# Kernel tuning notes

Measured on AMD Instinct MI355X. Metric: run time of the kernel, lower is better.

The kernel has to match this reference:

```python
import jax, jax.numpy as jnp
import numpy as np

DIM = 1024
N_HEADS = 16
HEAD_DIM = DIM // N_HEADS
SCALE = HEAD_DIM ** -0.5


def setup_inputs() -> dict:
    key = jax.random.key(0)
    kx, kq, kk, kv = jax.random.split(key, 4)
    x = jax.random.normal(kx, (2, 2048, DIM), dtype=jnp.float32)
    bv_q = jax.random.normal(kq, (N_HEADS, HEAD_DIM), dtype=jnp.float32) * 0.02
    bv_k = jax.random.normal(kk, (N_HEADS, HEAD_DIM), dtype=jnp.float32) * 0.02
    bv_v = jax.random.normal(kv, (N_HEADS, HEAD_DIM), dtype=jnp.float32) * 0.02
    return {"x": x, "bv_q": bv_q, "bv_k": bv_k, "bv_v": bv_v}


def reference(x, bv_q, bv_k, bv_v):
    B, T, D = x.shape
    H, HD = N_HEADS, HEAD_DIM
    x_h = x.reshape(B, T, H, HD)
    # sign-gated Q/K/V (sign of binding vectors; elementwise +/-1 gating)
    Q = x_h * jnp.sign(bv_q)  # [B,T,H,HD]
    K = x_h * jnp.sign(bv_k)
    V = x_h * jnp.sign(bv_v)
    # causal scores, sigmoid gating (no softmax)
    scores = jnp.einsum('bqhd,bkhd->bhqk', Q, K) * SCALE  # [B,H,T,T]
    causal = jnp.tril(jnp.ones((T, T), dtype=bool))
    attn = jnp.where(causal, jax.nn.sigmoid(scores * 4.0), 0.0)
    out = jnp.einsum('bhqk,bkhd->bqhd', attn, V)  # [B,T,H,HD]
    return out.reshape(B, T, D)
```

## Files before the change

kernel.cpp:

```cpp
#include <hip/hip_runtime.h>
#include <hip/hip_bf16.h>
#include <stdint.h>

#define DIM 1024
#define T_LEN 2048
#define NB 2
#define NH 16
#define HD 64
#define NQT 32

typedef float f32x4 __attribute__((ext_vector_type(4)));
typedef float f32x16 __attribute__((ext_vector_type(16)));
typedef __bf16 bf16x8 __attribute__((ext_vector_type(8)));
typedef __bf16 bf16x2 __attribute__((ext_vector_type(2)));
typedef unsigned int u32;
typedef unsigned int u32x4 __attribute__((ext_vector_type(4)));

__device__ __forceinline__ float sgnf(float v) {
    return (v > 0.f) ? 1.f : ((v < 0.f) ? -1.f : 0.f);
}

__device__ __forceinline__ float sigmoid_half(float v) {
    return __builtin_amdgcn_rcpf(1.f + __builtin_amdgcn_exp2f(-0.72134752f * v));
}

__device__ __forceinline__ u32 pack2(float p0, float p1) {
    bf16x2 t = {(__bf16)p0, (__bf16)p1};
    return __builtin_bit_cast(u32, t);
}

__device__ __forceinline__ void gload16(const __bf16* g, __bf16* l) {
    __builtin_amdgcn_global_load_lds(
        (__attribute__((address_space(1))) void*)g,
        (__attribute__((address_space(3))) void*)l,
        16, 0, 0);
}

__global__ __launch_bounds__(256) void prep_kernel(
    const float* __restrict__ x, __bf16* __restrict__ xb, __bf16* __restrict__ xt)
{
    __shared__ __align__(16) __bf16 tile[64][72];

    const int bid = blockIdx.x;
    const int h = bid & 15, tmp = bid >> 4, tt = tmp & 31, b = tmp >> 5;
    const int tid = threadIdx.x;
    const int r = tid >> 2, c0 = (tid & 3) * 16;

    const size_t rowbase = ((size_t)(b * T_LEN + tt * 64 + r)) * DIM + h * HD + c0;
    const float* xp = x + rowbase;

    __bf16 v[16];
    #pragma unroll
    for (int i = 0; i < 16; i += 4) {
        f32x4 f = *(const f32x4*)(xp + i);
        #pragma unroll
        for (int j = 0; j < 4; ++j) v[i + j] = (__bf16)f[j];
    }
    bf16x8 s0, s1;
    #pragma unroll
    for (int j = 0; j < 8; ++j) { s0[j] = v[j]; s1[j] = v[8 + j]; }
    *(bf16x8*)(xb + rowbase)     = s0;
    *(bf16x8*)(xb + rowbase + 8) = s1;
    *(bf16x8*)&tile[r][c0]     = s0;
    *(bf16x8*)&tile[r][c0 + 8] = s1;

    __syncthreads();

    const int d = tid >> 2, t0c = (tid & 3) * 16;
    __bf16 ov[16];
    #pragma unroll
    for (int i = 0; i < 16; ++i) ov[i] = tile[t0c + i][d];
    bf16x8 o0, o1;
    #pragma unroll
    for (int j = 0; j < 8; ++j) { o0[j] = ov[j]; o1[j] = ov[8 + j]; }
    const size_t obase = ((size_t)((b * NH + h) * HD + d)) * T_LEN + tt * 64 + t0c;
    *(bf16x8*)(xt + obase)     = o0;
    *(bf16x8*)(xt + obase + 8) = o1;
}

__global__ __launch_bounds__(256, 4) void mba_main(
    const __bf16* __restrict__ xb, const __bf16* __restrict__ xt,
    const float* __restrict__ bvq, const float* __restrict__ bvk,
    const float* __restrict__ bvv, float* __restrict__ out)
{
    __shared__ __align__(16) __bf16 Kb[3][64][64];
    __shared__ __align__(16) __bf16 Vb[2][64][64];

    const int bid = blockIdx.x;
    const int u = bid >> 5;
    const int jj = u >> 3, aa = u & 7;
    const int qt = 8 * jj + ((jj & 1) ? (7 - aa) : aa);
    const int bh = bid & 31;
    const int b = bh >> 4, h = bh & 15;
    const int q0 = qt * 64;

    const int tid = threadIdx.x;
    const int w = tid >> 6, l = tid & 63;
    const int c = l & 31, hi = l >> 5;
    const int qh = w & 1, sh = w >> 1;

    const size_t xb_bh = (size_t)b * T_LEN * DIM + h * HD;
    const size_t xt_bh = (size_t)((b * NH + h) * HD) * T_LEN;

    const int rr = l >> 3;
    const int sw = ((l & 7) ^ rr) << 3;

    auto STAGE_K = [&](int buf, int kvt) {
        const int kv0s = kvt * 64;
        #pragma unroll
        for (int pt = 0; pt < 2; ++pt) {
            const int r0 = w * 8 + pt * 32;
            gload16(xb + xb_bh + (size_t)(kv0s + r0 + rr) * DIM + sw, &Kb[buf][r0][0]);
        }
    };
    auto STAGE_V = [&](int buf, int kvt) {
        const int kv0s = kvt * 64;
        #pragma unroll
        for (int pt = 0; pt < 2; ++pt) {
            const int r0 = w * 8 + pt * 32;
            gload16(xt + xt_bh + (size_t)(r0 + rr) * T_LEN + kv0s + sw, &Vb[buf][r0][0]);
        }
    };

    STAGE_K(0, 0);
    STAGE_V(0, 0);
    if (qt >= 1) STAGE_K(1, 1);

    bf16x8 qa[4];
    {
        const float* bq = bvq + h * HD;
        const float* bk = bvk + h * HD;
        const int qrow = q0 + qh * 32 + c;
        #pragma unroll
        for (int m = 0; m < 4; ++m) {
            const int d0 = m * 16 + hi * 8;
            bf16x8 va = *(const bf16x8*)(xb + xb_bh + (size_t)qrow * DIM + d0);
            #pragma unroll
            for (int j = 0; j < 8; ++j) {
                float f = sgnf(bq[d0 + j]) * sgnf(bk[d0 + j]);
                qa[m][j] = (__bf16)((float)va[j] * f);
            }
        }
    }
    float sv[2];
    #pragma unroll
    for (int nd = 0; nd < 2; ++nd) sv[nd] = sgnf(bvv[h * HD + nd * 32 + c]);

    f32x16 o[2];
    #pragma unroll
    for (int nd = 0; nd < 2; ++nd)
        #pragma unroll
        for (int i = 0; i < 16; ++i) o[nd][i] = 0.f;

    int cur = 0;
    const int krow = sh * 32 + c;
    const int swz = (c & 7) << 4;

    for (int t = 0; t <= qt; ++t) {
        const bool last = (t == qt);
        if (last) { asm volatile("s_waitcnt vmcnt(0)" ::: "memory"); }
        else      { asm volatile("s_waitcnt vmcnt(2)" ::: "memory"); }
        __builtin_amdgcn_sched_barrier(0);
        __builtin_amdgcn_s_barrier();
        __builtin_amdgcn_sched_barrier(0);

        if (t + 1 <= qt) STAGE_V((t + 1) & 1, t + 1);
        __builtin_amdgcn_sched_barrier(0);
        if (t + 2 <= qt) {
            int stg = cur + 2; if (stg >= 3) stg -= 3;
            STAGE_K(stg, t + 2);
        }
        __builtin_amdgcn_sched_barrier(0);

        f32x16 ss;
        #pragma unroll
        for (int i = 0; i < 16; ++i) ss[i] = 0.f;
        #pragma unroll
        for (int m = 0; m < 4; ++m) {
            bf16x8 kf = *(const bf16x8*)((const char*)&Kb[cur][krow][0]
                          + ((m * 32 + hi * 16) ^ swz));
            ss = __builtin_amdgcn_mfma_f32_32x32x16_bf16(kf, qa[m], ss, 0, 0, 0);
        }

        u32 W[8];
        #pragma unroll
        for (int i = 0; i < 8; ++i) {
            const int r0 = 2 * i;
            const int sl = (r0 & 3) + 8 * (r0 >> 2) + 4 * hi;
            float p0 = sigmoid_half(ss[r0]);
            float p1 = sigmoid_half(ss[r0 + 1]);
            if (last) {
                const int sg = sh * 32 + sl;
                const int qg = qh * 32 + c;
                if (sg > qg)     p0 = 0.f;
                if (sg + 1 > qg) p1 = 0.f;
            }
            W[i] = pack2(p0, p1);
        }

        asm volatile("v_permlane32_swap_b32 %0, %1" : "+v"(W[0]), "+v"(W[2]));
        asm volatile("v_permlane32_swap_b32 %0, %1" : "+v"(W[1]), "+v"(W[3]));
        asm volatile("v_permlane32_swap_b32 %0, %1" : "+v"(W[4]), "+v"(W[6]));
        asm volatile("v_permlane32_swap_b32 %0, %1" : "+v"(W[5]), "+v"(W[7]));
        bf16x8 pa[2];
        pa[0] = __builtin_bit_cast(bf16x8, (u32x4){W[0], W[1], W[2], W[3]});
        pa[1] = __builtin_bit_cast(bf16x8, (u32x4){W[4], W[5], W[6], W[7]});

        #pragma unroll
        for (int m = 0; m < 2; ++m) {
            #pragma unroll
            for (int nd = 0; nd < 2; ++nd) {
                bf16x8 vf = *(const bf16x8*)((const char*)&Vb[t & 1][nd * 32 + c][0]
                              + ((sh * 64 + m * 32 + hi * 16) ^ swz));
                o[nd] = __builtin_amdgcn_mfma_f32_32x32x16_bf16(pa[m], vf, o[nd], 0, 0, 0);
            }
        }
        cur = (cur == 2) ? 0 : cur + 1;
    }

    __syncthreads();
    float (*osc)[64] = (float(*)[64]) & Kb[0][0][0];

    if (sh == 1) {
        #pragma unroll
        for (int r = 0; r < 16; ++r) {
            const int qloc = (r & 3) + 8 * (r >> 2) + 4 * hi;
            #pragma unroll
            for (int nd = 0; nd < 2; ++nd)
                osc[qh * 32 + qloc][nd * 32 + c] = o[nd][r];
        }
    }
    __syncthreads();
    if (sh == 0) {
        #pragma unroll
        for (int r = 0; r < 16; ++r) {
            const int qloc = (r & 3) + 8 * (r >> 2) + 4 * hi;
            const size_t row = (size_t)(b * T_LEN + q0 + qh * 32 + qloc) * DIM + h * HD;
            #pragma unroll
            for (int nd = 0; nd < 2; ++nd) {
                float val = (o[nd][r] + osc[qh * 32 + qloc][nd * 32 + c]) * sv[nd];
                out[row + nd * 32 + c] = val;
            }
        }
    }
}

__global__ __launch_bounds__(256) void mba_fallback(
    const float* __restrict__ x,
    const float* __restrict__ bvq,
    const float* __restrict__ bvk,
    const float* __restrict__ bvv,
    float* __restrict__ out)
{
    __shared__ __align__(16) __bf16 Kb[64][72];
    __shared__ __align__(16) __bf16 Vt[HD][72];
    __shared__ __align__(16) __bf16 Pb[4][16][72];

    const int bid = blockIdx.x;
    const int qt  = (NQT - 1) - (bid & (NQT - 1));
    const int bh  = bid >> 5;
    const int b   = bh >> 4;
    const int h   = bh & 15;

    const int tid = threadIdx.x;
    const int w   = tid >> 6;
    const int l   = tid & 63;
    const int lq  = l & 15;
    const int lh  = l >> 4;

    const int  q0    = qt * 64;
    const long xbase = ((long)b * T_LEN) * DIM + h * HD;

    bf16x8 qa[2];
    {
        const int   qrow = q0 + w * 16 + lq;
        const float* qp  = x + xbase + (long)qrow * DIM + lh * 8;
        const float* gp  = bvq + h * HD + lh * 8;
        #pragma unroll
        for (int ks = 0; ks < 2; ++ks)
            #pragma unroll
            for (int j = 0; j < 8; ++j)
                qa[ks][j] = (__bf16)(qp[ks * 32 + j] * sgnf(gp[ks * 32 + j]));
    }

    f32x4 o[4];
    #pragma unroll
    for (int n = 0; n < 4; ++n) o[n] = (f32x4){0.f, 0.f, 0.f, 0.f};

    const int r_st = tid >> 2;
    const int c0   = (tid & 3) * 16;
    const float* gk = bvk + h * HD + c0;
    const float* gv = bvv + h * HD + c0;

    for (int kvt = 0; kvt <= qt; ++kvt) {
        const int kv0 = kvt * 64;
        __syncthreads();
        {
            const float* kp = x + xbase + (long)(kv0 + r_st) * DIM + c0;
            __bf16 kb[16];
            #pragma unroll
            for (int i = 0; i < 16; ++i) kb[i] = (__bf16)(kp[i] * sgnf(gk[i]));
            *(bf16x8*)&Kb[r_st][c0]     = *(bf16x8*)&kb[0];
            *(bf16x8*)&Kb[r_st][c0 + 8] = *(bf16x8*)&kb[8];
            #pragma unroll
            for (int i = 0; i < 16; ++i)
                Vt[c0 + i][r_st] = (__bf16)(kp[i] * sgnf(gv[i]));
        }
        __syncthreads();

        f32x4 s[4];
        #pragma unroll
        for (int n = 0; n < 4; ++n) s[n] = (f32x4){0.f, 0.f, 0.f, 0.f};
        #pragma unroll
        for (int ks = 0; ks < 2; ++ks)
            #pragma unroll
            for (int n = 0; n < 4; ++n) {
                bf16x8 kf = *(const bf16x8*)&Kb[n * 16 + lq][ks * 32 + lh * 8];
                s[n] = __builtin_amdgcn_mfma_f32_16x16x32_bf16(qa[ks], kf, s[n], 0, 0, 0);
            }

        const bool diag = (kvt == qt);
        #pragma unroll
        for (int n = 0; n < 4; ++n)
            #pragma unroll
            for (int j = 0; j < 4; ++j) {
                float p = sigmoid_half(s[n][j]);
                if (diag && (n * 16 + lq) > (w * 16 + lh * 4 + j)) p = 0.f;
                Pb[w][lh * 4 + j][n * 16 + lq] = (__bf16)p;
            }

        #pragma unroll
        for (int ks = 0; ks < 2; ++ks) {
            bf16x8 pf = *(const bf16x8*)&Pb[w][lq][ks * 32 + lh * 8];
            #pragma unroll
            for (int n = 0; n < 4; ++n) {
                bf16x8 vf = *(const bf16x8*)&Vt[n * 16 + lq][ks * 32 + lh * 8];
                o[n] = __builtin_amdgcn_mfma_f32_16x16x32_bf16(pf, vf, o[n], 0, 0, 0);
            }
        }
    }

    float* op = out + ((long)b * T_LEN + q0 + w * 16) * DIM + h * HD;
    #pragma unroll
    for (int n = 0; n < 4; ++n)
        #pragma unroll
        for (int j = 0; j < 4; ++j)
            op[(long)(lh * 4 + j) * DIM + n * 16 + lq] = o[n][j];
}

extern "C" void kernel_launch(void* const* d_in, const int* in_sizes, int n_in,
                              void* d_out, int out_size, void* d_ws, size_t ws_size,
                              hipStream_t stream) {
    (void)in_sizes; (void)n_in; (void)out_size;
    const float* x   = (const float*)d_in[0];
    const float* bvq = (const float*)d_in[1];
    const float* bvk = (const float*)d_in[2];
    const float* bvv = (const float*)d_in[3];
    float* out = (float*)d_out;

    const size_t XB_BYTES = (size_t)NB * T_LEN * DIM * sizeof(__bf16);
    const size_t XT_BYTES = XB_BYTES;

    if (ws_size < XB_BYTES + XT_BYTES) {
        mba_fallback<<<NB * NH * NQT, 256, 0, stream>>>(x, bvq, bvk, bvv, out);
        return;
    }

    __bf16* xb = (__bf16*)d_ws;
    __bf16* xt = xb + (size_t)NB * T_LEN * DIM;

    prep_kernel<<<NB * NQT * NH, 256, 0, stream>>>(x, xb, xt);
    mba_main<<<NB * NH * NQT, 256, 0, stream>>>(xb, xt, bvq, bvk, bvv, out);
}
```

Baseline: 47.43 us.

## Split causal KV range into 4-tile chunks with atomic output accumulation

Each block now handles at most four KV tiles of one query tile rather than the whole causal prefix, so block work is balanced and 144 chunks per (b,h) are launched. Partial results are merged with float atomic adds into an output zeroed by a memset. The V sign gating moves into the prep kernel's transposed copy, and the in-block LDS reduction between the two key halves is dropped in favour of atomics. This trades the long-tail imbalance of the diagonal schedule for extra atomic traffic, a memset, and repeated Q loads per chunk.

```diff
diff --git a/kernel.cpp b/kernel.cpp
--- a/kernel.cpp
+++ b/kernel.cpp
@@ -8,6 +8,7 @@
 #define NH 16
 #define HD 64
 #define NQT 32
+#define NCHUNK 144
 
 typedef float f32x4 __attribute__((ext_vector_type(4)));
 typedef float f32x16 __attribute__((ext_vector_type(16)));
@@ -37,7 +38,8 @@
 }
 
 __global__ __launch_bounds__(256) void prep_kernel(
-    const float* __restrict__ x, __bf16* __restrict__ xb, __bf16* __restrict__ xt)
+    const float* __restrict__ x, const float* __restrict__ bvv,
+    __bf16* __restrict__ xb, __bf16* __restrict__ xt)
 {
     __shared__ __align__(16) __bf16 tile[64][72];
 
@@ -67,9 +69,10 @@
     __syncthreads();
 
     const int d = tid >> 2, t0c = (tid & 3) * 16;
+    const float g = sgnf(bvv[h * HD + d]);
     __bf16 ov[16];
     #pragma unroll
-    for (int i = 0; i < 16; ++i) ov[i] = tile[t0c + i][d];
+    for (int i = 0; i < 16; ++i) ov[i] = (__bf16)((float)tile[t0c + i][d] * g);
     bf16x8 o0, o1;
     #pragma unroll
     for (int j = 0; j < 8; ++j) { o0[j] = ov[j]; o1[j] = ov[8 + j]; }
@@ -81,15 +84,18 @@
 __global__ __launch_bounds__(256, 4) void mba_main(
     const __bf16* __restrict__ xb, const __bf16* __restrict__ xt,
     const float* __restrict__ bvq, const float* __restrict__ bvk,
-    const float* __restrict__ bvv, float* __restrict__ out)
+    float* __restrict__ out)
 {
     __shared__ __align__(16) __bf16 Kb[3][64][64];
     __shared__ __align__(16) __bf16 Vb[2][64][64];
 
     const int bid = blockIdx.x;
-    const int u = bid >> 5;
-    const int jj = u >> 3, aa = u & 7;
-    const int qt = 8 * jj + ((jj & 1) ? (7 - aa) : aa);
+    int rem = bid >> 5;
+    int qt = 31;
+    while (rem >= ((qt + 4) >> 2)) { rem -= (qt + 4) >> 2; --qt; }
+    const int c4 = rem * 4;
+    const int CL = min(4, qt + 1 - c4);
+
     const int bh = bid & 31;
     const int b = bh >> 4, h = bh & 15;
     const int q0 = qt * 64;
@@ -122,9 +128,9 @@
         }
     };
 
-    STAGE_K(0, 0);
-    STAGE_V(0, 0);
-    if (qt >= 1) STAGE_K(1, 1);
+    STAGE_K(0, c4);
+    STAGE_V(0, c4);
+    if (CL >= 2) STAGE_K(1, c4 + 1);
 
     bf16x8 qa[4];
     {
@@ -142,9 +148,6 @@
             }
         }
     }
-    float sv[2];
-    #pragma unroll
-    for (int nd = 0; nd < 2; ++nd) sv[nd] = sgnf(bvv[h * HD + nd * 32 + c]);
 
     f32x16 o[2];
     #pragma unroll
@@ -156,19 +159,21 @@
     const int krow = sh * 32 + c;
     const int swz = (c & 7) << 4;
 
-    for (int t = 0; t <= qt; ++t) {
-        const bool last = (t == qt);
-        if (last) { asm volatile("s_waitcnt vmcnt(0)" ::: "memory"); }
-        else      { asm volatile("s_waitcnt vmcnt(2)" ::: "memory"); }
+    for (int lt = 0; lt < CL; ++lt) {
+        const int gt = c4 + lt;
+        const bool last_local = (lt == CL - 1);
+        const bool diag = (gt == qt);
+        if (last_local) { asm volatile("s_waitcnt vmcnt(0)" ::: "memory"); }
+        else            { asm volatile("s_waitcnt vmcnt(2)" ::: "memory"); }
         __builtin_amdgcn_sched_barrier(0);
         __builtin_amdgcn_s_barrier();
         __builtin_amdgcn_sched_barrier(0);
 
-        if (t + 1 <= qt) STAGE_V((t + 1) & 1, t + 1);
+        if (lt + 1 < CL) STAGE_V((lt + 1) & 1, gt + 1);
         __builtin_amdgcn_sched_barrier(0);
-        if (t + 2 <= qt) {
+        if (lt + 2 < CL) {
             int stg = cur + 2; if (stg >= 3) stg -= 3;
-            STAGE_K(stg, t + 2);
+            STAGE_K(stg, gt + 2);
         }
         __builtin_amdgcn_sched_barrier(0);
 
@@ -189,7 +194,7 @@
             const int sl = (r0 & 3) + 8 * (r0 >> 2) + 4 * hi;
             float p0 = sigmoid_half(ss[r0]);
             float p1 = sigmoid_half(ss[r0 + 1]);
-            if (last) {
+            if (diag) {
                 const int sg = sh * 32 + sl;
                 const int qg = qh * 32 + c;
                 if (sg > qg)     p0 = 0.f;
@@ -210,7 +215,7 @@
         for (int m = 0; m < 2; ++m) {
             #pragma unroll
             for (int nd = 0; nd < 2; ++nd) {
-                bf16x8 vf = *(const bf16x8*)((const char*)&Vb[t & 1][nd * 32 + c][0]
+                bf16x8 vf = *(const bf16x8*)((const char*)&Vb[lt & 1][nd * 32 + c][0]
                               + ((sh * 64 + m * 32 + hi * 16) ^ swz));
                 o[nd] = __builtin_amdgcn_mfma_f32_32x32x16_bf16(pa[m], vf, o[nd], 0, 0, 0);
             }
@@ -218,30 +223,12 @@
         cur = (cur == 2) ? 0 : cur + 1;
     }
 
-    __syncthreads();
-    float (*osc)[64] = (float(*)[64]) & Kb[0][0][0];
-
-    if (sh == 1) {
-        #pragma unroll
-        for (int r = 0; r < 16; ++r) {
-            const int qloc = (r & 3) + 8 * (r >> 2) + 4 * hi;
-            #pragma unroll
-            for (int nd = 0; nd < 2; ++nd)
-                osc[qh * 32 + qloc][nd * 32 + c] = o[nd][r];
-        }
-    }
-    __syncthreads();
-    if (sh == 0) {
-        #pragma unroll
-        for (int r = 0; r < 16; ++r) {
-            const int qloc = (r & 3) + 8 * (r >> 2) + 4 * hi;
-            const size_t row = (size_t)(b * T_LEN + q0 + qh * 32 + qloc) * DIM + h * HD;
-            #pragma unroll
-            for (int nd = 0; nd < 2; ++nd) {
-                float val = (o[nd][r] + osc[qh * 32 + qloc][nd * 32 + c]) * sv[nd];
-                out[row + nd * 32 + c] = val;
-            }
-        }
+    #pragma unroll
+    for (int r = 0; r < 16; ++r) {
+        const int qloc = (r & 3) + 8 * (r >> 2) + 4 * hi;
+        float* op = out + (size_t)(b * T_LEN + q0 + qh * 32 + qloc) * DIM + h * HD + c;
+        unsafeAtomicAdd(op,      o[0][r]);
+        unsafeAtomicAdd(op + 32, o[1][r]);
     }
 }
 
@@ -351,7 +338,7 @@
 extern "C" void kernel_launch(void* const* d_in, const int* in_sizes, int n_in,
                               void* d_out, int out_size, void* d_ws, size_t ws_size,
                               hipStream_t stream) {
-    (void)in_sizes; (void)n_in; (void)out_size;
+    (void)in_sizes; (void)n_in;
     const float* x   = (const float*)d_in[0];
     const float* bvq = (const float*)d_in[1];
     const float* bvk = (const float*)d_in[2];
@@ -369,6 +356,7 @@
     __bf16* xb = (__bf16*)d_ws;
     __bf16* xt = xb + (size_t)NB * T_LEN * DIM;
 
-    prep_kernel<<<NB * NQT * NH, 256, 0, stream>>>(x, xb, xt);
-    mba_main<<<NB * NH * NQT, 256, 0, stream>>>(xb, xt, bvq, bvk, bvv, out);
-}
+    hipMemsetAsync(d_out, 0, (size_t)out_size * sizeof(float), stream);
+    prep_kernel<<<NB * NQT * NH, 256, 0, stream>>>(x, bvv, xb, xt);
+    mba_main<<<NCHUNK * 32, 256, 0, stream>>>(xb, xt, bvq, bvk, out);
+}
```

New measurement: 141.8 us. 2.99x slower.

## Pair complementary causal query tiles per block to share K/V staging

Applied to the files above, without the earlier changes.

Each block now processes two query tiles (qt and 31-qt) for the same batch-head, so every block does equal causal work and shares each staged K/V tile between both tiles' MFMAs. The grid is halved to 512 blocks and launch bounds relaxed to 2 waves per SIMD to make room for doubled accumulator registers. The V sign gating is folded into the prep transpose, which removes the per-output multiply. This trades occupancy and parallelism for load balance and halved K/V traffic.

```diff
diff --git a/kernel.cpp b/kernel.cpp
--- a/kernel.cpp
+++ b/kernel.cpp
@@ -37,7 +37,8 @@
 }
 
 __global__ __launch_bounds__(256) void prep_kernel(
-    const float* __restrict__ x, __bf16* __restrict__ xb, __bf16* __restrict__ xt)
+    const float* __restrict__ x, const float* __restrict__ bvv,
+    __bf16* __restrict__ xb, __bf16* __restrict__ xt)
 {
     __shared__ __align__(16) __bf16 tile[64][72];
 
@@ -67,9 +68,10 @@
     __syncthreads();
 
     const int d = tid >> 2, t0c = (tid & 3) * 16;
+    const float g = sgnf(bvv[h * HD + d]);
     __bf16 ov[16];
     #pragma unroll
-    for (int i = 0; i < 16; ++i) ov[i] = tile[t0c + i][d];
+    for (int i = 0; i < 16; ++i) ov[i] = (__bf16)((float)tile[t0c + i][d] * g);
     bf16x8 o0, o1;
     #pragma unroll
     for (int j = 0; j < 8; ++j) { o0[j] = ov[j]; o1[j] = ov[8 + j]; }
@@ -78,21 +80,20 @@
     *(bf16x8*)(xt + obase + 8) = o1;
 }
 
-__global__ __launch_bounds__(256, 4) void mba_main(
+__global__ __launch_bounds__(256, 2) void mba_main(
     const __bf16* __restrict__ xb, const __bf16* __restrict__ xt,
     const float* __restrict__ bvq, const float* __restrict__ bvk,
-    const float* __restrict__ bvv, float* __restrict__ out)
+    float* __restrict__ out)
 {
     __shared__ __align__(16) __bf16 Kb[3][64][64];
     __shared__ __align__(16) __bf16 Vb[2][64][64];
 
     const int bid = blockIdx.x;
-    const int u = bid >> 5;
-    const int jj = u >> 3, aa = u & 7;
-    const int qt = 8 * jj + ((jj & 1) ? (7 - aa) : aa);
+    const int p = bid >> 5;
     const int bh = bid & 31;
     const int b = bh >> 4, h = bh & 15;
-    const int q0 = qt * 64;
+    const int qtA = 31 - p, qtB = p;
+    const int q0A = qtA * 64, q0B = qtB * 64;
 
     const int tid = threadIdx.x;
     const int w = tid >> 6, l = tid & 63;
@@ -124,87 +125,92 @@
 
     STAGE_K(0, 0);
     STAGE_V(0, 0);
-    if (qt >= 1) STAGE_K(1, 1);
-
-    bf16x8 qa[4];
+    STAGE_K(1, 1);
+
+    bf16x8 qaA[4], qaB[4];
     {
         const float* bq = bvq + h * HD;
         const float* bk = bvk + h * HD;
-        const int qrow = q0 + qh * 32 + c;
         #pragma unroll
         for (int m = 0; m < 4; ++m) {
             const int d0 = m * 16 + hi * 8;
-            bf16x8 va = *(const bf16x8*)(xb + xb_bh + (size_t)qrow * DIM + d0);
+            bf16x8 va = *(const bf16x8*)(xb + xb_bh + (size_t)(q0A + qh * 32 + c) * DIM + d0);
+            bf16x8 vb = *(const bf16x8*)(xb + xb_bh + (size_t)(q0B + qh * 32 + c) * DIM + d0);
             #pragma unroll
             for (int j = 0; j < 8; ++j) {
                 float f = sgnf(bq[d0 + j]) * sgnf(bk[d0 + j]);
-                qa[m][j] = (__bf16)((float)va[j] * f);
-            }
-        }
-    }
-    float sv[2];
-    #pragma unroll
-    for (int nd = 0; nd < 2; ++nd) sv[nd] = sgnf(bvv[h * HD + nd * 32 + c]);
-
-    f32x16 o[2];
+                qaA[m][j] = (__bf16)((float)va[j] * f);
+                qaB[m][j] = (__bf16)((float)vb[j] * f);
+            }
+        }
+    }
+
+    f32x16 oA[2], oB[2];
     #pragma unroll
     for (int nd = 0; nd < 2; ++nd)
         #pragma unroll
-        for (int i = 0; i < 16; ++i) o[nd][i] = 0.f;
+        for (int i = 0; i < 16; ++i) { oA[nd][i] = 0.f; oB[nd][i] = 0.f; }
 
     int cur = 0;
     const int krow = sh * 32 + c;
     const int swz = (c & 7) << 4;
 
-    for (int t = 0; t <= qt; ++t) {
-        const bool last = (t == qt);
+    auto makeP = [&](const f32x16& ss, bool diag, bf16x8* pa) {
+        u32 W[8];
+        #pragma unroll
+        for (int i = 0; i < 8; ++i) {
+            const int r0 = 2 * i;
+            const int sl = (r0 & 3) + 8 * (r0 >> 2) + 4 * hi;
+            float p0 = sigmoid_half(ss[r0]);
+            float p1 = sigmoid_half(ss[r0 + 1]);
+            if (diag) {
+                const int sg = sh * 32 + sl;
+                const int qg = qh * 32 + c;
+                if (sg > qg)     p0 = 0.f;
+                if (sg + 1 > qg) p1 = 0.f;
+            }
+            W[i] = pack2(p0, p1);
+        }
+        asm volatile("v_permlane32_swap_b32 %0, %1" : "+v"(W[0]), "+v"(W[2]));
+        asm volatile("v_permlane32_swap_b32 %0, %1" : "+v"(W[1]), "+v"(W[3]));
+        asm volatile("v_permlane32_swap_b32 %0, %1" : "+v"(W[4]), "+v"(W[6]));
+        asm volatile("v_permlane32_swap_b32 %0, %1" : "+v"(W[5]), "+v"(W[7]));
+        pa[0] = __builtin_bit_cast(bf16x8, (u32x4){W[0], W[1], W[2], W[3]});
+        pa[1] = __builtin_bit_cast(bf16x8, (u32x4){W[4], W[5], W[6], W[7]});
+    };
+
+    for (int t = 0; t <= qtA; ++t) {
+        const bool last = (t == qtA);
+        const bool dual = (t <= qtB);
         if (last) { asm volatile("s_waitcnt vmcnt(0)" ::: "memory"); }
         else      { asm volatile("s_waitcnt vmcnt(2)" ::: "memory"); }
         __builtin_amdgcn_sched_barrier(0);
         __builtin_amdgcn_s_barrier();
         __builtin_amdgcn_sched_barrier(0);
 
-        if (t + 1 <= qt) STAGE_V((t + 1) & 1, t + 1);
+        if (t + 1 <= qtA) STAGE_V((t + 1) & 1, t + 1);
         __builtin_amdgcn_sched_barrier(0);
-        if (t + 2 <= qt) {
+        if (t + 2 <= qtA) {
             int stg = cur + 2; if (stg >= 3) stg -= 3;
             STAGE_K(stg, t + 2);
         }
         __builtin_amdgcn_sched_barrier(0);
 
-        f32x16 ss;
-        #pragma unroll
-        for (int i = 0; i < 16; ++i) ss[i] = 0.f;
+        f32x16 ssA, ssB;
+        #pragma unroll
+        for (int i = 0; i < 16; ++i) { ssA[i] = 0.f; ssB[i] = 0.f; }
         #pragma unroll
         for (int m = 0; m < 4; ++m) {
             bf16x8 kf = *(const bf16x8*)((const char*)&Kb[cur][krow][0]
                           + ((m * 32 + hi * 16) ^ swz));
-            ss = __builtin_amdgcn_mfma_f32_32x32x16_bf16(kf, qa[m], ss, 0, 0, 0);
-        }
-
-        u32 W[8];
-        #pragma unroll
-        for (int i = 0; i < 8; ++i) {
-            const int r0 = 2 * i;
-            const int sl = (r0 & 3) + 8 * (r0 >> 2) + 4 * hi;
-            float p0 = sigmoid_half(ss[r0]);
-            float p1 = sigmoid_half(ss[r0 + 1]);
-            if (last) {
-                const int sg = sh * 32 + sl;
-                const int qg = qh * 32 + c;
-                if (sg > qg)     p0 = 0.f;
-                if (sg + 1 > qg) p1 = 0.f;
-            }
-            W[i] = pack2(p0, p1);
-        }
-
-        asm volatile("v_permlane32_swap_b32 %0, %1" : "+v"(W[0]), "+v"(W[2]));
-        asm volatile("v_permlane32_swap_b32 %0, %1" : "+v"(W[1]), "+v"(W[3]));
-        asm volatile("v_permlane32_swap_b32 %0, %1" : "+v"(W[4]), "+v"(W[6]));
-        asm volatile("v_permlane32_swap_b32 %0, %1" : "+v"(W[5]), "+v"(W[7]));
-        bf16x8 pa[2];
-        pa[0] = __builtin_bit_cast(bf16x8, (u32x4){W[0], W[1], W[2], W[3]});
-        pa[1] = __builtin_bit_cast(bf16x8, (u32x4){W[4], W[5], W[6], W[7]});
+            ssA = __builtin_amdgcn_mfma_f32_32x32x16_bf16(kf, qaA[m], ssA, 0, 0, 0);
+            if (dual)
+                ssB = __builtin_amdgcn_mfma_f32_32x32x16_bf16(kf, qaB[m], ssB, 0, 0, 0);
+        }
+
+        bf16x8 paA[2], paB[2];
+        makeP(ssA, last, paA);
+        if (dual) makeP(ssB, t == qtB, paB);
 
         #pragma unroll
         for (int m = 0; m < 2; ++m) {
@@ -212,7 +218,9 @@
             for (int nd = 0; nd < 2; ++nd) {
                 bf16x8 vf = *(const bf16x8*)((const char*)&Vb[t & 1][nd * 32 + c][0]
                               + ((sh * 64 + m * 32 + hi * 16) ^ swz));
-                o[nd] = __builtin_amdgcn_mfma_f32_32x32x16_bf16(pa[m], vf, o[nd], 0, 0, 0);
+                oA[nd] = __builtin_amdgcn_mfma_f32_32x32x16_bf16(paA[m], vf, oA[nd], 0, 0, 0);
+                if (dual)
+                    oB[nd] = __builtin_amdgcn_mfma_f32_32x32x16_bf16(paB[m], vf, oB[nd], 0, 0, 0);
             }
         }
         cur = (cur == 2) ? 0 : cur + 1;
@@ -225,9 +233,8 @@
         #pragma unroll
         for (int r = 0; r < 16; ++r) {
             const int qloc = (r & 3) + 8 * (r >> 2) + 4 * hi;
-            #pragma unroll
-            for (int nd = 0; nd < 2; ++nd)
-                osc[qh * 32 + qloc][nd * 32 + c] = o[nd][r];
+            osc[qh * 32 + qloc][c]      = oA[0][r];
+            osc[qh * 32 + qloc][32 + c] = oA[1][r];
         }
     }
     __syncthreads();
@@ -235,12 +242,28 @@
         #pragma unroll
         for (int r = 0; r < 16; ++r) {
             const int qloc = (r & 3) + 8 * (r >> 2) + 4 * hi;
-            const size_t row = (size_t)(b * T_LEN + q0 + qh * 32 + qloc) * DIM + h * HD;
-            #pragma unroll
-            for (int nd = 0; nd < 2; ++nd) {
-                float val = (o[nd][r] + osc[qh * 32 + qloc][nd * 32 + c]) * sv[nd];
-                out[row + nd * 32 + c] = val;
-            }
+            const size_t row = (size_t)(b * T_LEN + q0A + qh * 32 + qloc) * DIM + h * HD;
+            out[row + c]      = oA[0][r] + osc[qh * 32 + qloc][c];
+            out[row + 32 + c] = oA[1][r] + osc[qh * 32 + qloc][32 + c];
+        }
+    }
+    __syncthreads();
+    if (sh == 1) {
+        #pragma unroll
+        for (int r = 0; r < 16; ++r) {
+            const int qloc = (r & 3) + 8 * (r >> 2) + 4 * hi;
+            osc[qh * 32 + qloc][c]      = oB[0][r];
+            osc[qh * 32 + qloc][32 + c] = oB[1][r];
+        }
+    }
+    __syncthreads();
+    if (sh == 0) {
+        #pragma unroll
+        for (int r = 0; r < 16; ++r) {
+            const int qloc = (r & 3) + 8 * (r >> 2) + 4 * hi;
+            const size_t row = (size_t)(b * T_LEN + q0B + qh * 32 + qloc) * DIM + h * HD;
+            out[row + c]      = oB[0][r] + osc[qh * 32 + qloc][c];
+            out[row + 32 + c] = oB[1][r] + osc[qh * 32 + qloc][32 + c];
         }
     }
 }
@@ -369,6 +392,6 @@
     __bf16* xb = (__bf16*)d_ws;
     __bf16* xt = xb + (size_t)NB * T_LEN * DIM;
 
-    prep_kernel<<<NB * NQT * NH, 256, 0, stream>>>(x, xb, xt);
-    mba_main<<<NB * NH * NQT, 256, 0, stream>>>(xb, xt, bvq, bvk, bvv, out);
-}
+    prep_kernel<<<NB * NQT * NH, 256, 0, stream>>>(x, bvv, xb, xt);
+    mba_main<<<16 * 32, 256, 0, stream>>>(xb, xt, bvq, bvk, out);
+}
```

New measurement: 52.94 us. 11.6% more time.
